# Performance work log

Hardware: AMD Instinct MI355X
Metric: run time of the kernel (lower is better)

The kernel has to match this reference:

```python
import jax, jax.numpy as jnp
import numpy as np

N, K, D = 500_000, 256, 64  # points, prototypes, feature dim


def setup_inputs() -> dict:
    key = jax.random.key(0)
    kx, km = jax.random.split(key)
    X = jax.random.normal(kx, (N, D), dtype=jnp.float32)
    mus = jax.random.normal(km, (K, D), dtype=jnp.float32)
    return {"X": X, "mus": mus}


def reference(X, mus):
    # Faithful to vmap(lambda x: argmin(sum((mus - x)**2, axis=1)))(X),
    # but expressed with the Gram-matrix distance trick so the K*D broadcast
    # is a single GEMM instead of an O(N,K,D) elementwise intermediate.
    x_sq = jnp.sum(X * X, axis=1, keepdims=True)        # [N, 1]
    mu_sq = jnp.sum(mus * mus, axis=1)                  # [K]
    d2 = x_sq - 2.0 * (X @ mus.T) + mu_sq[None, :]      # [N, K] squared dists
    return jnp.argmin(d2, axis=1)                       # [N] int assignments
```

## Files before the change

kernel.cpp:

```cpp
#include <hip/hip_runtime.h>


#define DIM 64
#define NPROTO 256
#define NBLK 1024
#define MARGIN_ACC 0.017f

using f32x4 = __attribute__((ext_vector_type(4))) float;
using f16x8 = __attribute__((ext_vector_type(8))) _Float16;

__device__ __forceinline__ f16x8 cvt8(float4 a, float4 b) {
    f16x8 r;
    r[0] = (_Float16)a.x; r[1] = (_Float16)a.y;
    r[2] = (_Float16)a.z; r[3] = (_Float16)a.w;
    r[4] = (_Float16)b.x; r[5] = (_Float16)b.y;
    r[6] = (_Float16)b.z; r[7] = (_Float16)b.w;
    return r;
}

__global__ void __launch_bounds__(256)
argmin_mfma_kernel(const float* __restrict__ X,
                   const float* __restrict__ mus,
                   int* __restrict__ out,
                   unsigned* __restrict__ ws_count,
                   int* __restrict__ ws_list,
                   int use_list, int n) {
    __shared__ __align__(16) f16x8 s_frag[16][2][64];
    __shared__ __align__(16) float s_seed[NPROTO];

    const int tid = threadIdx.x;
    const int w = tid >> 6;
    const int l = tid & 63;
    const int lp = l & 15;
    const int lg = l >> 4;

#pragma unroll
    for (int pp = 0; pp < 4; ++pp) {
        const int p = w * 4 + pp;
        const float* src = mus + (size_t)(p * 16 + lp) * DIM + lg * 8;
        const float4 a = *(const float4*)(src);
        const float4 b = *(const float4*)(src + 4);
        const float4 c = *(const float4*)(src + 32);
        const float4 d = *(const float4*)(src + 36);
        s_frag[p][0][l] = cvt8(a, b);
        s_frag[p][1][l] = cvt8(c, d);
        float s = 0.f;
        s = fmaf(a.x, a.x, fmaf(a.y, a.y, fmaf(a.z, a.z, fmaf(a.w, a.w, s))));
        s = fmaf(b.x, b.x, fmaf(b.y, b.y, fmaf(b.z, b.z, fmaf(b.w, b.w, s))));
        s = fmaf(c.x, c.x, fmaf(c.y, c.y, fmaf(c.z, c.z, fmaf(c.w, c.w, s))));
        s = fmaf(d.x, d.x, fmaf(d.y, d.y, fmaf(d.z, d.z, fmaf(d.w, d.w, s))));
        s += __shfl_xor(s, 16);
        s += __shfl_xor(s, 32);
        if (lg == 0) s_seed[p * 16 + lp] = -0.5f * s;
    }
    __syncthreads();

    const int ngroups = (n + 15) / 16;
    const int NW = NBLK * 4;
    const int gwid = blockIdx.x * 4 + w;
    const int q = ngroups / NW, rr = ngroups % NW;
    const int g0 = gwid * q + (gwid < rr ? gwid : rr);
    const int cnt = q + (gwid < rr ? 1 : 0);

    const int kofs = 255 - lg * 4;

    float4 xr0, xr1, xr2, xr3;
    if (cnt > 0) {
        int row = g0 * 16 + lp; row = (row < n) ? row : (n - 1);
        const float* rp = X + (size_t)row * DIM + lg * 8;
        xr0 = *(const float4*)(rp);
        xr1 = *(const float4*)(rp + 4);
        xr2 = *(const float4*)(rp + 32);
        xr3 = *(const float4*)(rp + 36);
    }

    for (int it = 0; it < cnt; ++it) {
        const int g = g0 + it;
        const bool more = (it + 1 < cnt);

        const f16x8 bx0 = cvt8(xr0, xr1);
        const f16x8 bx1 = cvt8(xr2, xr3);

        if (more) {
            int row = (g + 1) * 16 + lp; row = (row < n) ? row : (n - 1);
            const float* rp = X + (size_t)row * DIM + lg * 8;
            xr0 = *(const float4*)(rp);
            xr1 = *(const float4*)(rp + 4);
            xr2 = *(const float4*)(rp + 32);
            xr3 = *(const float4*)(rp + 36);
        }

        float b1 = -3.4e38f, b2 = -3.4e38f;
#pragma unroll
        for (int p = 0; p < 16; ++p) {
            const f16x8 A0 = s_frag[p][0][l];
            const f16x8 A1 = s_frag[p][1][l];
            const f32x4 seed = *(const f32x4*)&s_seed[p * 16 + lg * 4];
            f32x4 acc = __builtin_amdgcn_mfma_f32_16x16x32_f16(
                A0, bx0, seed, 0, 0, 0);
            acc = __builtin_amdgcn_mfma_f32_16x16x32_f16(A1, bx1, acc,
                                                         0, 0, 0);
            float pv[4];
#pragma unroll
            for (int r = 0; r < 4; ++r) {
                unsigned u = __float_as_uint(acc[r]);
                u = (u & 0xFFFFFF00u) + (unsigned)(kofs - p * 16 - r);
                pv[r] = __uint_as_float(u);
            }
            const float t1a = fmaxf(pv[0], pv[1]), t2a = fminf(pv[0], pv[1]);
            const float t1b = fmaxf(pv[2], pv[3]), t2b = fminf(pv[2], pv[3]);
            const float p1 = fmaxf(t1a, t1b);
            const float p2 = fmaxf(fminf(t1a, t1b), fmaxf(t2a, t2b));
            const float nb2 = fmaxf(fminf(b1, p1), fmaxf(b2, p2));
            b1 = fmaxf(b1, p1);
            b2 = nb2;
        }
#pragma unroll
        for (int m = 16; m <= 32; m <<= 1) {
            const float o1 = __shfl_xor(b1, m);
            const float o2 = __shfl_xor(b2, m);
            const float nb2 = fmaxf(fminf(b1, o1), fmaxf(b2, o2));
            b1 = fmaxf(b1, o1);
            b2 = nb2;
        }

        bool fl = false;
        const int i = g * 16 + l;
        if (l < 16 && i < n) {
            const unsigned u1 = __float_as_uint(b1);
            const int k1 = 255 - (int)(u1 & 0xFFu);
            const float v1 = __uint_as_float(u1 & 0xFFFFFF00u);
            const float v2 =
                __uint_as_float(__float_as_uint(b2) & 0xFFFFFF00u);
            const bool close = (v1 - v2) < MARGIN_ACC;
            if (use_list) {
                out[i] = k1;
                fl = close;
            } else {
                out[i] = (int)((unsigned)k1 | (close ? 0x80000000u : 0u));
            }
        }
        if (use_list) {
            const unsigned long long mask = __ballot(fl);
            if (mask) {
                unsigned base = 0;
                if (l == 0)
                    base = atomicAdd(ws_count, (unsigned)__popcll(mask));
                base = __shfl(base, 0);
                if (fl)
                    ws_list[base + __popcll(mask & ((1ull << l) - 1))] = i;
            }
        }
    }
}

#define MSTRIDE 65

__global__ void __launch_bounds__(256)
fixup_lds_kernel(const float* __restrict__ X, const float* __restrict__ mus,
                 const unsigned* __restrict__ ws_count,
                 const int* __restrict__ ws_list, int* __restrict__ out) {
    __shared__ float s_mu[NPROTO * MSTRIDE];
    __shared__ float s_msq[NPROTO];

    const int tid = threadIdx.x;
    {
        const float4* mr = (const float4*)(mus + (size_t)tid * DIM);
        float q0 = 0.f, q1 = 0.f, q2 = 0.f, q3 = 0.f;
#pragma unroll
        for (int qq = 0; qq < 16; ++qq) {
            const float4 mv = mr[qq];
            const int base = tid * MSTRIDE + qq * 4;
            s_mu[base]     = mv.x;
            s_mu[base + 1] = mv.y;
            s_mu[base + 2] = mv.z;
            s_mu[base + 3] = mv.w;
            q0 = fmaf(mv.x, mv.x, q0);
            q1 = fmaf(mv.y, mv.y, q1);
            q2 = fmaf(mv.z, mv.z, q2);
            q3 = fmaf(mv.w, mv.w, q3);
        }
        s_msq[tid] = (q0 + q1) + (q2 + q3);
    }
    __syncthreads();

    const int l = tid & 63;
    const int gw = (int)((blockIdx.x * blockDim.x + tid) >> 6);
    const int NW = (int)((gridDim.x * blockDim.x) >> 6);
    const int nf = (int)*ws_count;

    for (int j = gw; j < nf; j += NW) {
        const int pt = ws_list[j];
        const float4* xr = (const float4*)(X + (size_t)pt * DIM);
        float4 xv[16];
        float a0 = 0.f, a1 = 0.f, a2 = 0.f, a3 = 0.f;
#pragma unroll
        for (int qq = 0; qq < 16; ++qq) {
            xv[qq] = xr[qq];
            a0 = fmaf(xv[qq].x, xv[qq].x, a0);
            a1 = fmaf(xv[qq].y, xv[qq].y, a1);
            a2 = fmaf(xv[qq].z, xv[qq].z, a2);
            a3 = fmaf(xv[qq].w, xv[qq].w, a3);
        }
        const float xsq = (a0 + a1) + (a2 + a3);
        float b1 = 3.4e38f;
        int k1 = 0;
#pragma unroll
        for (int e = 0; e < 4; ++e) {
            const int p = e * 64 + l;
            const float* mr = &s_mu[p * MSTRIDE];
            float d0 = 0.f, d1 = 0.f, d2 = 0.f, d3 = 0.f;
#pragma unroll
            for (int qq = 0; qq < 16; ++qq) {
                d0 = fmaf(mr[qq * 4],     xv[qq].x, d0);
                d1 = fmaf(mr[qq * 4 + 1], xv[qq].y, d1);
                d2 = fmaf(mr[qq * 4 + 2], xv[qq].z, d2);
                d3 = fmaf(mr[qq * 4 + 3], xv[qq].w, d3);
            }
            const float dot = (d0 + d1) + (d2 + d3);
            const float dd = (xsq - 2.0f * dot) + s_msq[p];
            if (dd < b1) { b1 = dd; k1 = p; }
        }
#pragma unroll
        for (int mm = 1; mm < 64; mm <<= 1) {
            const float ob = __shfl_xor(b1, mm);
            const int ok = __shfl_xor(k1, mm);
            if (ob < b1 || (ob == b1 && ok < k1)) { b1 = ob; k1 = ok; }
        }
        if (l == 0) out[pt] = k1;
    }
}

__global__ void __launch_bounds__(256)
fixup_scan_lds_kernel(const float* __restrict__ X,
                      const float* __restrict__ mus,
                      int* __restrict__ out, int n) {
    __shared__ float s_mu[NPROTO * MSTRIDE];
    __shared__ float s_msq[NPROTO];

    const int tid = threadIdx.x;
    {
        const float4* mr = (const float4*)(mus + (size_t)tid * DIM);
        float q0 = 0.f, q1 = 0.f, q2 = 0.f, q3 = 0.f;
#pragma unroll
        for (int qq = 0; qq < 16; ++qq) {
            const float4 mv = mr[qq];
            const int base = tid * MSTRIDE + qq * 4;
            s_mu[base]     = mv.x;
            s_mu[base + 1] = mv.y;
            s_mu[base + 2] = mv.z;
            s_mu[base + 3] = mv.w;
            q0 = fmaf(mv.x, mv.x, q0);
            q1 = fmaf(mv.y, mv.y, q1);
            q2 = fmaf(mv.z, mv.z, q2);
            q3 = fmaf(mv.w, mv.w, q3);
        }
        s_msq[tid] = (q0 + q1) + (q2 + q3);
    }
    __syncthreads();

    const int l = tid & 63;
    const int gw = (int)((blockIdx.x * blockDim.x + tid) >> 6);
    const int NW = (int)((gridDim.x * blockDim.x) >> 6);
    const int chunk = (n + NW - 1) / NW;
    const int base = gw * chunk;
    const int end = (base + chunk < n) ? (base + chunk) : n;

    for (int s = base; s < end; s += 64) {
        const int i = s + l;
        const int v = (i < end) ? out[i] : 0;
        const bool flg = (i < end) && ((unsigned)v & 0x80000000u);
        unsigned long long m = __ballot(flg);
        while (m) {
            const int src = (int)__ffsll((unsigned long long)m) - 1;
            m &= m - 1;
            const int pt = __shfl(i, src);
            const float4* xr = (const float4*)(X + (size_t)pt * DIM);
            float4 xv[16];
            float a0 = 0.f, a1 = 0.f, a2 = 0.f, a3 = 0.f;
#pragma unroll
            for (int qq = 0; qq < 16; ++qq) {
                xv[qq] = xr[qq];
                a0 = fmaf(xv[qq].x, xv[qq].x, a0);
                a1 = fmaf(xv[qq].y, xv[qq].y, a1);
                a2 = fmaf(xv[qq].z, xv[qq].z, a2);
                a3 = fmaf(xv[qq].w, xv[qq].w, a3);
            }
            const float xsq = (a0 + a1) + (a2 + a3);
            float b1 = 3.4e38f;
            int k1 = 0;
#pragma unroll
            for (int e = 0; e < 4; ++e) {
                const int p = e * 64 + l;
                const float* mr = &s_mu[p * MSTRIDE];
                float d0 = 0.f, d1 = 0.f, d2 = 0.f, d3 = 0.f;
#pragma unroll
                for (int qq = 0; qq < 16; ++qq) {
                    d0 = fmaf(mr[qq * 4],     xv[qq].x, d0);
                    d1 = fmaf(mr[qq * 4 + 1], xv[qq].y, d1);
                    d2 = fmaf(mr[qq * 4 + 2], xv[qq].z, d2);
                    d3 = fmaf(mr[qq * 4 + 3], xv[qq].w, d3);
                }
                const float dot = (d0 + d1) + (d2 + d3);
                const float dd = (xsq - 2.0f * dot) + s_msq[p];
                if (dd < b1) { b1 = dd; k1 = p; }
            }
#pragma unroll
            for (int mm = 1; mm < 64; mm <<= 1) {
                const float ob = __shfl_xor(b1, mm);
                const int ok = __shfl_xor(k1, mm);
                if (ob < b1 || (ob == b1 && ok < k1)) { b1 = ob; k1 = ok; }
            }
            if (l == 0) out[pt] = k1;
        }
    }
}

extern "C" void kernel_launch(void* const* d_in, const int* in_sizes, int n_in,
                              void* d_out, int out_size, void* d_ws, size_t ws_size,
                              hipStream_t stream) {
    const float* X = (const float*)d_in[0];
    const float* mus = (const float*)d_in[1];
    int* out = (int*)d_out;
    const int n = in_sizes[0] / DIM;

    unsigned* ws_count = (unsigned*)d_ws;
    int* ws_list = (int*)((char*)d_ws + 16);
    const int use_list = (ws_size >= 16 + (size_t)n * 4) ? 1 : 0;

    if (use_list) {
        hipMemsetAsync(d_ws, 0, 16, stream);
    }

    argmin_mfma_kernel<<<NBLK, 256, 0, stream>>>(X, mus, out, ws_count,
                                                 ws_list, use_list, n);
    if (use_list) {
        fixup_lds_kernel<<<512, 256, 0, stream>>>(X, mus, ws_count, ws_list,
                                                  out);
    } else {
        fixup_scan_lds_kernel<<<512, 256, 0, stream>>>(X, mus, out, n);
    }
}
```

Measured before the change: 76.19 us.

## Process two 16-row groups per wave iteration to reuse prototype fragments

Each wave iteration now handles 32 points as two independent 16-row MFMA tiles. The same LDS prototype fragments and seed bias feed both tiles, which halves the LDS reads per point. The two independent MFMA chains and running top-2 reductions also give the scheduler more work to overlap. The cost is more VGPRs for the doubled X prefetch and accumulators, and fewer iterations per wave for spreading load across the grid.

```diff
diff --git a/kernel.cpp b/kernel.cpp
--- a/kernel.cpp
+++ b/kernel.cpp
@@ -55,7 +55,7 @@
     }
     __syncthreads();
 
-    const int ngroups = (n + 15) / 16;
+    const int ngroups = (n + 31) / 32;
     const int NW = NBLK * 4;
     const int gwid = blockIdx.x * 4 + w;
     const int q = ngroups / NW, rr = ngroups % NW;
@@ -64,74 +64,98 @@
 
     const int kofs = 255 - lg * 4;
 
-    float4 xr0, xr1, xr2, xr3;
+    float4 xa0, xa1, xa2, xa3, xb0, xb1, xb2, xb3;
     if (cnt > 0) {
-        int row = g0 * 16 + lp; row = (row < n) ? row : (n - 1);
-        const float* rp = X + (size_t)row * DIM + lg * 8;
-        xr0 = *(const float4*)(rp);
-        xr1 = *(const float4*)(rp + 4);
-        xr2 = *(const float4*)(rp + 32);
-        xr3 = *(const float4*)(rp + 36);
+        int rA = g0 * 32 + lp;      rA = (rA < n) ? rA : (n - 1);
+        int rB = g0 * 32 + 16 + lp; rB = (rB < n) ? rB : (n - 1);
+        const float* pA = X + (size_t)rA * DIM + lg * 8;
+        const float* pB = X + (size_t)rB * DIM + lg * 8;
+        xa0 = *(const float4*)(pA);      xa1 = *(const float4*)(pA + 4);
+        xa2 = *(const float4*)(pA + 32); xa3 = *(const float4*)(pA + 36);
+        xb0 = *(const float4*)(pB);      xb1 = *(const float4*)(pB + 4);
+        xb2 = *(const float4*)(pB + 32); xb3 = *(const float4*)(pB + 36);
     }
 
     for (int it = 0; it < cnt; ++it) {
         const int g = g0 + it;
         const bool more = (it + 1 < cnt);
 
-        const f16x8 bx0 = cvt8(xr0, xr1);
-        const f16x8 bx1 = cvt8(xr2, xr3);
+        const f16x8 bxA0 = cvt8(xa0, xa1), bxA1 = cvt8(xa2, xa3);
+        const f16x8 bxB0 = cvt8(xb0, xb1), bxB1 = cvt8(xb2, xb3);
 
         if (more) {
-            int row = (g + 1) * 16 + lp; row = (row < n) ? row : (n - 1);
-            const float* rp = X + (size_t)row * DIM + lg * 8;
-            xr0 = *(const float4*)(rp);
-            xr1 = *(const float4*)(rp + 4);
-            xr2 = *(const float4*)(rp + 32);
-            xr3 = *(const float4*)(rp + 36);
-        }
-
-        float b1 = -3.4e38f, b2 = -3.4e38f;
+            int rA = (g + 1) * 32 + lp;      rA = (rA < n) ? rA : (n - 1);
+            int rB = (g + 1) * 32 + 16 + lp; rB = (rB < n) ? rB : (n - 1);
+            const float* pA = X + (size_t)rA * DIM + lg * 8;
+            const float* pB = X + (size_t)rB * DIM + lg * 8;
+            xa0 = *(const float4*)(pA);      xa1 = *(const float4*)(pA + 4);
+            xa2 = *(const float4*)(pA + 32); xa3 = *(const float4*)(pA + 36);
+            xb0 = *(const float4*)(pB);      xb1 = *(const float4*)(pB + 4);
+            xb2 = *(const float4*)(pB + 32); xb3 = *(const float4*)(pB + 36);
+        }
+
+        float b1A = -3.4e38f, b2A = -3.4e38f;
+        float b1B = -3.4e38f, b2B = -3.4e38f;
 #pragma unroll
         for (int p = 0; p < 16; ++p) {
             const f16x8 A0 = s_frag[p][0][l];
             const f16x8 A1 = s_frag[p][1][l];
             const f32x4 seed = *(const f32x4*)&s_seed[p * 16 + lg * 4];
-            f32x4 acc = __builtin_amdgcn_mfma_f32_16x16x32_f16(
-                A0, bx0, seed, 0, 0, 0);
-            acc = __builtin_amdgcn_mfma_f32_16x16x32_f16(A1, bx1, acc,
-                                                         0, 0, 0);
-            float pv[4];
-#pragma unroll
-            for (int r = 0; r < 4; ++r) {
-                unsigned u = __float_as_uint(acc[r]);
-                u = (u & 0xFFFFFF00u) + (unsigned)(kofs - p * 16 - r);
-                pv[r] = __uint_as_float(u);
-            }
-            const float t1a = fmaxf(pv[0], pv[1]), t2a = fminf(pv[0], pv[1]);
-            const float t1b = fmaxf(pv[2], pv[3]), t2b = fminf(pv[2], pv[3]);
-            const float p1 = fmaxf(t1a, t1b);
-            const float p2 = fmaxf(fminf(t1a, t1b), fmaxf(t2a, t2b));
-            const float nb2 = fmaxf(fminf(b1, p1), fmaxf(b2, p2));
-            b1 = fmaxf(b1, p1);
-            b2 = nb2;
+            f32x4 accA = __builtin_amdgcn_mfma_f32_16x16x32_f16(
+                A0, bxA0, seed, 0, 0, 0);
+            f32x4 accB = __builtin_amdgcn_mfma_f32_16x16x32_f16(
+                A0, bxB0, seed, 0, 0, 0);
+            accA = __builtin_amdgcn_mfma_f32_16x16x32_f16(A1, bxA1, accA,
+                                                          0, 0, 0);
+            accB = __builtin_amdgcn_mfma_f32_16x16x32_f16(A1, bxB1, accB,
+                                                          0, 0, 0);
+#pragma unroll
+            for (int gg = 0; gg < 2; ++gg) {
+                const f32x4 acc = gg ? accB : accA;
+                float pv[4];
+#pragma unroll
+                for (int r = 0; r < 4; ++r) {
+                    unsigned u = __float_as_uint(acc[r]);
+                    u = (u & 0xFFFFFF00u) + (unsigned)(kofs - p * 16 - r);
+                    pv[r] = __uint_as_float(u);
+                }
+                const float t1a = fmaxf(pv[0], pv[1]);
+                const float t2a = fminf(pv[0], pv[1]);
+                const float t1b = fmaxf(pv[2], pv[3]);
+                const float t2b = fminf(pv[2], pv[3]);
+                const float p1 = fmaxf(t1a, t1b);
+                const float p2 = fmaxf(fminf(t1a, t1b), fmaxf(t2a, t2b));
+                if (gg) {
+                    const float nb2 = fmaxf(fminf(b1B, p1), fmaxf(b2B, p2));
+                    b1B = fmaxf(b1B, p1);
+                    b2B = nb2;
+                } else {
+                    const float nb2 = fmaxf(fminf(b1A, p1), fmaxf(b2A, p2));
+                    b1A = fmaxf(b1A, p1);
+                    b2A = nb2;
+                }
+            }
         }
 #pragma unroll
         for (int m = 16; m <= 32; m <<= 1) {
-            const float o1 = __shfl_xor(b1, m);
-            const float o2 = __shfl_xor(b2, m);
-            const float nb2 = fmaxf(fminf(b1, o1), fmaxf(b2, o2));
-            b1 = fmaxf(b1, o1);
-            b2 = nb2;
+            const float o1A = __shfl_xor(b1A, m), o2A = __shfl_xor(b2A, m);
+            const float o1B = __shfl_xor(b1B, m), o2B = __shfl_xor(b2B, m);
+            const float n2A = fmaxf(fminf(b1A, o1A), fmaxf(b2A, o2A));
+            const float n2B = fmaxf(fminf(b1B, o1B), fmaxf(b2B, o2B));
+            b1A = fmaxf(b1A, o1A); b2A = n2A;
+            b1B = fmaxf(b1B, o1B); b2B = n2B;
         }
 
         bool fl = false;
-        const int i = g * 16 + l;
-        if (l < 16 && i < n) {
-            const unsigned u1 = __float_as_uint(b1);
+        const int i = g * 32 + l;
+        if (l < 32 && i < n) {
+            const float f1 = (l < 16) ? b1A : b1B;
+            const float f2 = (l < 16) ? b2A : b2B;
+            const unsigned u1 = __float_as_uint(f1);
             const int k1 = 255 - (int)(u1 & 0xFFu);
             const float v1 = __uint_as_float(u1 & 0xFFFFFF00u);
             const float v2 =
-                __uint_as_float(__float_as_uint(b2) & 0xFFFFFF00u);
+                __uint_as_float(__float_as_uint(f2) & 0xFFFFFF00u);
             const bool close = (v1 - v2) < MARGIN_ACC;
             if (use_list) {
                 out[i] = k1;
```

New measurement: 79.30 us. +4.1%, slower.
